# Kernel optimization log

Hardware: AMD Instinct MI355X
Metric: run time of the kernel (lower is better)

Reference implementation:

```python
import jax, jax.numpy as jnp
import numpy as np

B, P, K = 8, 1024, 20
N = B * P
EMB, OUT = 1024, 40
GRID = 5

def _window(W):
    # Hamming taper (window_type='hamming')
    n = jnp.arange(W, dtype=jnp.float32)
    return 0.54 - 0.46 * jnp.cos(2.0 * jnp.pi * n / (W - 1))

def _init_kan(key, din, dout, W, S, g):
    nw = (din - W) // S + 1
    coeffs = jax.random.normal(key, (2, dout, nw, W, g), jnp.float32) / (np.sqrt(nw * W) * np.sqrt(g))
    bias = jnp.zeros((dout,), jnp.float32)
    return coeffs, bias

def stft_kan(x, coeffs, bias, W, S):
    # x: (n, D) -> (n, dout). Slice D into overlapping windows of size W,
    # stride S, apply Hamming taper, build Fourier features cos(k*x), sin(k*x)
    # for k=1..g and contract with learned coefficients (STFT-Fourier-KAN).
    nw, g = coeffs.shape[2], coeffs.shape[4]
    idx = (np.arange(nw) * S)[:, None] + np.arange(W)[None, :]        # (nw, W)
    xw = x[:, idx] * _window(W)                                        # (n, nw, W)
    kfreq = jnp.arange(1, g + 1, dtype=x.dtype)
    arg = xw[..., None] * kfreq                                        # (n, nw, W, g)
    y = (jnp.einsum('nwig,owig->no', jnp.cos(arg), coeffs[0])
         + jnp.einsum('nwig,owig->no', jnp.sin(arg), coeffs[1]))
    return y + bias

def setup_inputs():
    key = jax.random.key(0)
    ks = jax.random.split(key, 5)
    pos = jax.random.normal(ks[0], (N, 3), jnp.float32)
    batch = (jnp.arange(N) // P).astype(jnp.int32)  # sorted, equal-size clouds
    c1, b1 = _init_kan(ks[1], 6, 64, 3, 3, GRID)
    c2, b2 = _init_kan(ks[2], 64, 128, 16, 8, GRID)
    c3, b3 = _init_kan(ks[3], 128, EMB, 32, 16, GRID)
    c4, b4 = _init_kan(ks[4], 2 * EMB, OUT, 256, 128, GRID)
    return {"pos": pos, "batch": batch, "c1": c1, "b1": b1, "c2": c2, "b2": b2,
            "c3": c3, "b3": b3, "c4": c4, "b4": b4}

def reference(pos, batch, c1, b1, c2, b2, c3, b3, c4, b4):
    posb = pos.reshape(B, P, 3)
    # dynamic kNN graph per cloud (self excluded)
    d = jnp.sum((posb[:, :, None, :] - posb[:, None, :, :]) ** 2, -1)  # (B,P,P)
    d = d + jnp.eye(P, dtype=d.dtype) * 1e10
    _, nbr = jax.lax.top_k(-d, K)                                      # (B,P,K)
    pj = jax.vmap(lambda p, i: p[i])(posb, nbr)                        # (B,P,K,3)
    pi = jnp.broadcast_to(posb[:, :, None, :], pj.shape)
    e = jnp.concatenate([pi, pj - pi], -1).reshape(N * K, 6)           # edge feats
    h = stft_kan(e, c1, b1, 3, 3)                                      # (N*K,64)
    h = stft_kan(h, c2, b2, 16, 8)                                     # (N*K,128)
    x1 = jnp.max(h.reshape(N, K, 128), axis=1)                         # max aggr over neighbors
    x = stft_kan(x1, c3, b3, 32, 16)                                   # (N,EMB)
    gmax = jax.ops.segment_max(x, batch, num_segments=B)
    gsum = jax.ops.segment_sum(x, batch, num_segments=B)
    cnt = jax.ops.segment_sum(jnp.ones((N, 1), x.dtype), batch, num_segments=B)
    xg = jnp.concatenate([gmax, gsum / cnt], -1)                       # (B, 2*EMB)
    return stft_kan(xg, c4, b4, 256, 128)                              # (B, OUT)
```

## Files before the change

kernel.cpp:

```cpp
#include <hip/hip_runtime.h>


typedef unsigned short u16;
typedef unsigned int   u32;
typedef unsigned long long u64;
typedef __attribute__((ext_vector_type(8))) _Float16 half8;
typedef __attribute__((ext_vector_type(4))) float f32x4;

__device__ __forceinline__ float bf2f(u16 u) {
  u32 v = ((u32)u) << 16;
  return __uint_as_float(v);
}
__device__ __forceinline__ u16 f2bfr(float f) {
  u32 x = __float_as_uint(f);
  u32 r = x + 0x7FFFu + ((x >> 16) & 1u);
  return (u16)(r >> 16);
}
__device__ __forceinline__ u16 f2h(float f) {
  _Float16 h = (_Float16)f;
  u16 r;
  __builtin_memcpy(&r, &h, 2);
  return r;
}
__device__ __forceinline__ float h2f(u16 u) {
  _Float16 h;
  __builtin_memcpy(&h, &u, 2);
  return (float)h;
}
__device__ __forceinline__ float ldf(const void* p, size_t i, bool f32) {
  return f32 ? ((const float*)p)[i] : bf2f(((const u16*)p)[i]);
}
__device__ __forceinline__ u64 minu64(u64 a, u64 b) { return a < b ? a : b; }

#define NBR_OFF   ((size_t)0)
#define FLAG_OFF  ((size_t)917504)
#define XG_OFF    ((size_t)(1u << 20))
#define L4P_OFF   (((size_t)(1u << 20)) + 131072)
#define C1T_OFF   (((size_t)(1u << 20)) + 524288)
#define C2T_OFF   (((size_t)(1u << 20)) + 589824)
#define C3T_OFF   ((size_t)(2u << 20))
#define C4T_OFF   ((size_t)(7u << 20))
#define PMAX_OFF  ((size_t)(13u << 20))
#define PSUM_OFF  ((size_t)(14u << 20))
#define X1_OFF    ((size_t)(15u << 20))
#define H1_OFF    ((size_t)(18u << 20))

__global__ void detect_kernel(const void* __restrict__ pos,
                              int* __restrict__ flag) {
  int t = threadIdx.x;
  float a = fabsf(((const float*)pos)[t]);
  bool ok = (a > 1.0e-3f && a < 100.0f);
  unsigned long long m = __ballot(ok);
  if (t == 0) *flag = (__popcll(m) >= 32) ? 1 : 0;
}

__global__ void tkan_all_kernel(const void* __restrict__ s1, void* __restrict__ d1,
                                const void* __restrict__ s2, void* __restrict__ d2,
                                const void* __restrict__ s3, void* __restrict__ d3,
                                const void* __restrict__ s4, void* __restrict__ d4,
                                const int* __restrict__ dfl) {
  const int blk = blockIdx.x;
  const void* src; void* dst;
  int dout, nw, W, total, KPAD, outf32, base;
  if (blk < 16)        { src = s1; dst = d1; dout = 64;   nw = 2;  W = 3;
                         total = 64 * 64;     KPAD = 64;    outf32 = 0; base = 0; }
  else if (blk < 576)  { src = s2; dst = d2; dout = 128;  nw = 7;  W = 16;
                         total = 128 * 1120;  KPAD = 1120;  outf32 = 0; base = 16; }
  else if (blk < 9536) { src = s3; dst = d3; dout = 1024; nw = 7;  W = 32;
                         total = 1024 * 2240; KPAD = 2240;  outf32 = 0; base = 576; }
  else                 { src = s4; dst = d4; dout = 40;   nw = 15; W = 256;
                         total = 40 * 38400;  KPAD = 38400; outf32 = 1; base = 9536; }
  int id = (blk - base) * 256 + threadIdx.x;
  if (id >= total) return;
  const bool f32 = (*dfl != 0);
  int o = id / KPAD, f = id % KPAD;
  int NA = nw * W;
  int Kt = NA * 10;
  float v = 0.f;
  if (f < Kt) {
    int part = f & 1, p = f >> 1;
    int aa, gg;
    if (p < 4 * NA) { aa = p >> 2;      gg = p & 3; }
    else            { aa = p - 4 * NA;  gg = 4;     }
    int i = aa % W, w = aa / W;
    int OS = NA * 5;
    size_t sidx = (size_t)part * (dout * OS) + (size_t)o * OS + w * (W * 5) + i * 5 + gg;
    v = ldf(src, sidx, f32);
  }
  if (outf32) ((float*)dst)[id] = v;
  else        ((u16*)dst)[id] = f2h(v);
}

__global__ __launch_bounds__(256) void knn_kernel(const void* __restrict__ pos,
                                                  int* __restrict__ nbr,
                                                  const int* __restrict__ dfl) {
  __shared__ float px[1024], py[1024], pz[1024];
  const bool f32 = (*dfl != 0);
  const int t = threadIdx.x;
  const int b = blockIdx.y;
  const int base = b << 10;
  for (int j = t; j < 1024; j += 256) {
    size_t pidx = (size_t)(base + j) * 3;
    px[j] = ldf(pos, pidx, f32);
    py[j] = ldf(pos, pidx + 1, f32);
    pz[j] = ldf(pos, pidx + 2, f32);
  }
  __syncthreads();
  const int wv = t >> 6, lane = t & 63;
  const int q = blockIdx.x * 4 + wv;
  const float qx = px[q], qy = py[q], qz = pz[q];
  u64 key[16];
#pragma unroll
  for (int s = 0; s < 16; ++s) {
    const int j = s * 64 + lane;
    float dx = qx - px[j], dy = qy - py[j], dz = qz - pz[j];
    float d = __fadd_rn(__fadd_rn(__fmul_rn(dx, dx), __fmul_rn(dy, dy)),
                        __fmul_rn(dz, dz));
    key[s] = (j == q) ? ~0ull
                      : ((((u64)__float_as_uint(d)) << 32) | (u32)j);
  }
  const int obase = (base + q) * 20;
  for (int k = 0; k < 20; ++k) {
    u64 m = key[0];
#pragma unroll
    for (int s = 1; s < 16; ++s) m = minu64(m, key[s]);
#pragma unroll
    for (int off = 32; off >= 1; off >>= 1) {
      u32 lo = (u32)m, hi = (u32)(m >> 32);
      lo = __shfl_xor(lo, off, 64);
      hi = __shfl_xor(hi, off, 64);
      m = minu64(m, (((u64)hi) << 32) | lo);
    }
    if (lane == 0) nbr[obase + k] = (int)(u32)m;
#pragma unroll
    for (int s = 0; s < 16; ++s)
      if (key[s] == m) key[s] = ~0ull;
  }
}

template <int L>
__global__ __launch_bounds__(256, 3) void kan_kernel(
    const void* __restrict__ in_, const int* __restrict__ nbr,
    const void* __restrict__ pos, const u16* __restrict__ ct,
    const void* __restrict__ bias, void* __restrict__ out_,
    float* __restrict__ pmax, float* __restrict__ psum,
    const int* __restrict__ dfl) {
  constexpr int W    = (L == 1) ? 3  : (L == 2) ? 16  : 32;
  constexpr int S    = (L == 1) ? 3  : (L == 2) ? 8   : 16;
  constexpr int DIN  = (L == 1) ? 6  : (L == 2) ? 64  : 128;
  constexpr int NT   = 64;
  constexpr int NW   = (DIN - W) / S + 1;
  constexpr int NA   = NW * W;
  constexpr int NPAIR = NA * 5;
  constexpr int S1P  = NA * 4;
  constexpr int KROW  = (L == 1) ? 64 : NPAIR * 2;
  constexpr int NCH   = KROW / 32;
  constexpr int NB    = NT / 16;
  constexpr int RW    = (L == 1) ? 64 : (L == 2) ? 80 : 32;
  constexpr int MB    = RW / 16;
  constexpr int PSTH  = DIN + 4;
  constexpr int LGW   = (W == 16) ? 4 : 5;
  constexpr int BBS   = 4 * 520;

  __shared__ float hamS[(L == 1) ? 1 : W];
  __shared__ float wT1[(L == 1) ? 32 : 1];
  __shared__ int   hT1[(L == 1) ? 32 : 1];
  __shared__ u16   slab[(L == 1) ? 2 : 4 * RW * PSTH];
  __shared__ u16   stage1[(L == 1) ? 4 * 64 * 64 : 2];
  __shared__ u16   Bbuf[2 * BBS];

  const bool f32 = (*dfl != 0);
  const u16* inH = (const u16*)in_;
  const int t = threadIdx.x;
  if constexpr (L == 1) {
    if (t < 32) {
      float wv_ = 0.f; int hx = 0;
      if (t < NPAIR) {
        int aa, gg;
        if (t < S1P) { aa = t >> 2;   gg = t & 3; }
        else         { aa = t - S1P;  gg = 4;     }
        int i = aa % W;
        float hm = 0.54f - 0.46f * cospif(2.0f * (float)i / (float)(W - 1));
        wv_ = hm * (float)(gg + 1);
        hx = aa;
      }
      wT1[t] = wv_; hT1[t] = hx;
    }
  } else {
    if (t < W) hamS[t] = 0.54f - 0.46f * cospif(2.0f * (float)t / (float)(W - 1));
  }

  int tile, ncol0;
  if constexpr (L == 3) {
    const int id = blockIdx.x;
    tile = (id >> 3) & 63;
    ncol0 = ((((id & 7) << 1) | (id >> 9))) * NT;
  } else {
    tile = blockIdx.x;
    ncol0 = blockIdx.y * NT;
  }
  const int lane = t & 63, wv = t >> 6;
  const int m16 = lane & 15, kb = lane >> 4;
  const int rowbase = tile * (4 * RW) + wv * RW;
  u16* myslab = &slab[(L == 1) ? 0 : wv * RW * PSTH];

  const int scol = t >> 2, spart = t & 3;
  const u16* srcB = ct + (size_t)(ncol0 + scol) * KROW + spart * 8;

  if constexpr (L >= 2) {
    constexpr int F4R = DIN / 4;
    constexpr int TOT = RW * F4R;
    for (int i = lane; i < TOT; i += 64) {
      const int r = i / F4R, c4 = i % F4R;
      *(uint2*)(myslab + r * PSTH + c4 * 4) =
          *(const uint2*)(inH + (size_t)(rowbase + r) * DIN + c4 * 4);
    }
  }

  {
    const uint4 v = *(const uint4*)srcB;
    *(uint4*)(Bbuf + spart * 520 + scol * 8) = v;
  }
  __syncthreads();

  f32x4 acc[MB][NB];
#pragma unroll
  for (int mb = 0; mb < MB; ++mb)
#pragma unroll
    for (int nb = 0; nb < NB; ++nb) {
      acc[mb][nb][0] = 0.f; acc[mb][nb][1] = 0.f;
      acc[mb][nb][2] = 0.f; acc[mb][nb][3] = 0.f;
    }

  for (int c = 0; c < NCH; ++c) {
    uint4 bnext;
    const bool havenext = (c + 1 < NCH);
    if (havenext)
      bnext = *(const uint4*)(srcB + (c + 1) * 32);
    const int pg0 = c * 16 + kb * 4;
    half8 af[MB];
    if constexpr (L == 1) {
      float wm[4]; int hx[4]; bool val[4];
#pragma unroll
      for (int u = 0; u < 4; ++u) {
        const int pg = pg0 + u;
        wm[u] = wT1[pg]; hx[u] = hT1[pg]; val[u] = (pg < NPAIR);
      }
#pragma unroll
      for (int mb = 0; mb < MB; ++mb) {
        const int row = rowbase + mb * 16 + m16;
        const int pt = row / 20;
        const int cloud = pt >> 10, ci = pt & 1023;
        const int cb = cloud << 10;
        const int jl = nbr[row];
#pragma unroll
        for (int u = 0; u < 4; ++u) {
          float cs = 0.f, sn = 0.f;
          if (val[u]) {
            const int aa = hx[u];
            float v;
            if (aa < 3) {
              v = ldf(pos, (size_t)(cb + ci) * 3 + aa, f32);
            } else {
              const int cc2 = aa - 3;
              v = ldf(pos, (size_t)(cb + jl) * 3 + cc2, f32) -
                  ldf(pos, (size_t)(cb + ci) * 3 + cc2, f32);
            }
            const float ang = v * wm[u];
            cs = __cosf(ang); sn = __sinf(ang);
          }
          af[mb][2 * u]     = (_Float16)cs;
          af[mb][2 * u + 1] = (_Float16)sn;
        }
      }
    } else if (pg0 < S1P) {
      const int aa = pg0 >> 2;
      const int i = aa & (W - 1), w = aa >> LGW;
      const int hidx = S * w + i;
      const float hm = hamS[i];
#pragma unroll
      for (int mb = 0; mb < MB; ++mb) {
        const u16* rp = myslab + (mb * 16 + m16) * PSTH;
        const float th = h2f(rp[hidx]) * hm;
        const float c1 = __cosf(th), s1 = __sinf(th);
        const float tc = 2.0f * c1;
        const float c2 = tc * c1 - 1.0f, s2 = tc * s1;
        const float c3 = tc * c2 - c1,   s3 = tc * s2 - s1;
        const float c4 = tc * c3 - c2,   s4 = tc * s3 - s2;
        af[mb][0] = (_Float16)c1; af[mb][1] = (_Float16)s1;
        af[mb][2] = (_Float16)c2; af[mb][3] = (_Float16)s2;
        af[mb][4] = (_Float16)c3; af[mb][5] = (_Float16)s3;
        af[mb][6] = (_Float16)c4; af[mb][7] = (_Float16)s4;
      }
    } else {
      const int q0 = pg0 - S1P;
      float wm[4]; int hx[4];
#pragma unroll
      for (int u = 0; u < 4; ++u) {
        const int aa = q0 + u;
        const int i = aa & (W - 1), w = aa >> LGW;
        hx[u] = S * w + i;
        wm[u] = hamS[i] * 5.0f;
      }
#pragma unroll
      for (int mb = 0; mb < MB; ++mb) {
        const u16* rp = myslab + (mb * 16 + m16) * PSTH;
#pragma unroll
        for (int u = 0; u < 4; ++u) {
          const float ang = h2f(rp[hx[u]]) * wm[u];
          af[mb][2 * u]     = (_Float16)__cosf(ang);
          af[mb][2 * u + 1] = (_Float16)__sinf(ang);
        }
      }
    }
    const u16* bb = Bbuf + (c & 1) * BBS + kb * 520;
#pragma unroll
    for (int nb = 0; nb < NB; ++nb) {
      const half8 bv = *(const half8*)(bb + (nb * 16 + m16) * 8);
#pragma unroll
      for (int mb = 0; mb < MB; ++mb)
        acc[mb][nb] = __builtin_amdgcn_mfma_f32_16x16x32_f16(
            af[mb], bv, acc[mb][nb], 0, 0, 0);
    }
    if (havenext) {
      *(uint4*)(Bbuf + ((c + 1) & 1) * BBS + spart * 520 + scol * 8) = bnext;
      __syncthreads();
    }
  }

  if constexpr (L == 1) {
    u16* st = &stage1[wv * 4096];
#pragma unroll
    for (int mb = 0; mb < MB; ++mb)
#pragma unroll
      for (int nb = 0; nb < NB; ++nb) {
        const float bsv = ldf(bias, nb * 16 + m16, f32);
#pragma unroll
        for (int r = 0; r < 4; ++r)
          st[(mb * 16 + kb * 4 + r) * 64 + nb * 16 + m16] =
              f2h(acc[mb][nb][r] + bsv);
      }
    u16* gp = (u16*)out_ + (size_t)rowbase * 64;
    for (int i = lane; i < 512; i += 64)
      *(uint4*)(gp + i * 8) = *(const uint4*)&st[i * 8];
  } else if constexpr (L == 2) {
    u16* st = myslab;
#pragma unroll
    for (int mb = 0; mb < MB; ++mb)
#pragma unroll
      for (int nb = 0; nb < NB; ++nb) {
        const float bsv = ldf(bias, ncol0 + nb * 16 + m16, f32);
#pragma unroll
        for (int r = 0; r < 4; ++r)
          st[(mb * 16 + kb * 4 + r) * PSTH + nb * 16 + m16] =
              f2h(acc[mb][nb][r] + bsv);
      }
    const int pbase = tile * 16 + wv * 4;
#pragma unroll
    for (int j = 0; j < 4; ++j) {
      float m = -3.0e38f;
#pragma unroll
      for (int k = 0; k < 20; ++k)
        m = fmaxf(m, h2f(st[(j * 20 + k) * PSTH + lane]));
      ((u16*)out_)[(size_t)(pbase + j) * 128 + ncol0 + lane] = f2h(m);
    }
  } else {
    const int chunk = rowbase >> 5;
#pragma unroll
    for (int nb = 0; nb < NB; ++nb) {
      const int col = ncol0 + nb * 16 + m16;
      const float bsv = ldf(bias, col, f32);
      float m = -3.0e38f, s = 0.f;
#pragma unroll
      for (int mb = 0; mb < MB; ++mb)
#pragma unroll
        for (int r = 0; r < 4; ++r) {
          const float v = acc[mb][nb][r] + bsv;
          m = fmaxf(m, v); s += v;
        }
#pragma unroll
      for (int off = 16; off <= 32; off <<= 1) {
        m = fmaxf(m, __shfl_xor(m, off, 64));
        s += __shfl_xor(s, off, 64);
      }
      if (kb == 0) {
        pmax[(size_t)chunk * 1024 + col] = m;
        psum[(size_t)chunk * 1024 + col] = s;
      }
    }
  }
}

__global__ void seg2_kernel(const float* __restrict__ pmax,
                            const float* __restrict__ psum,
                            float* __restrict__ xg) {
  const int id = blockIdx.x * 256 + threadIdx.x;
  const int b = id >> 10, col = id & 1023;
  float m = -3.0e38f, s = 0.f;
  for (int rc = 0; rc < 32; ++rc) {
    m = fmaxf(m, pmax[(size_t)(b * 32 + rc) * 1024 + col]);
    s += psum[(size_t)(b * 32 + rc) * 1024 + col];
  }
  xg[b * 2048 + col] = m;
  xg[b * 2048 + 1024 + col] = s * (1.0f / 1024.0f);
}

__global__ __launch_bounds__(256) void l4_kernel(const float* __restrict__ xg,
                                                 const float* __restrict__ c4t,
                                                 float* __restrict__ part) {
  __shared__ float F[2560];
  const int t = threadIdx.x;
  const int w = blockIdx.x, b = blockIdx.y;
  const float xv = xg[b * 2048 + w * 128 + t];
  const float hm = 0.54f - 0.46f * cospif(2.0f * (float)t / 255.0f);
  const float aa = xv * hm;
  const float c1 = __cosf(aa), s1 = __sinf(aa);
  const float tc = 2.0f * c1;
  const float c2 = tc * c1 - 1.0f, s2 = tc * s1;
  const float c3 = tc * c2 - c1,   s3 = tc * s2 - s1;
  const float c4 = tc * c3 - c2,   s4 = tc * s3 - s2;
  const float a5 = aa * 5.0f;
  F[t * 8]     = c1; F[t * 8 + 1] = s1;
  F[t * 8 + 2] = c2; F[t * 8 + 3] = s2;
  F[t * 8 + 4] = c3; F[t * 8 + 5] = s3;
  F[t * 8 + 6] = c4; F[t * 8 + 7] = s4;
  F[2048 + t * 2]     = __cosf(a5);
  F[2048 + t * 2 + 1] = __sinf(a5);
  __syncthreads();
  if (t < 240) {
    const int o = t % 40, s = t / 40;
    const int f0 = s * 432;
    const int f1 = (f0 + 432 < 2560) ? (f0 + 432) : 2560;
    const float* cp1 = c4t + (size_t)o * 38400 + w * 2048;
    const float* cp2 = c4t + (size_t)o * 38400 + 30720 + w * 512;
    float acc = 0.f;
    for (int f = f0; f < f1; f += 4) {
      const float* cpf = (f < 2048) ? (cp1 + f) : (cp2 + (f - 2048));
      const float4 cv = *(const float4*)cpf;
      const float4 fa = *(const float4*)&F[f];
      acc += fa.x * cv.x + fa.y * cv.y + fa.z * cv.z + fa.w * cv.w;
    }
    part[((b * 15 + w) * 6 + s) * 40 + o] = acc;
  }
}

__global__ void outred_kernel(const float* __restrict__ part,
                              const void* __restrict__ b4,
                              void* __restrict__ outp,
                              const int* __restrict__ dfl) {
  int t = threadIdx.x;
  if (t >= 320) return;
  const bool f32 = (*dfl != 0);
  int b = t / 40, o = t % 40;
  float s = ldf(b4, o, f32);
  for (int w = 0; w < 15; ++w)
#pragma unroll
    for (int sl = 0; sl < 6; ++sl)
      s += part[((b * 15 + w) * 6 + sl) * 40 + o];
  if (f32) ((float*)outp)[t] = s;
  else     ((u16*)outp)[t] = f2bfr(s);
}

extern "C" void kernel_launch(void* const* d_in, const int* in_sizes, int n_in,
                              void* d_out, int out_size, void* d_ws,
                              size_t ws_size, hipStream_t stream) {
  (void)in_sizes; (void)n_in; (void)out_size; (void)ws_size;
  const void* pos = d_in[0];
  const void* c1 = d_in[2];
  const void* b1 = d_in[3];
  const void* c2 = d_in[4];
  const void* b2 = d_in[5];
  const void* c3 = d_in[6];
  const void* b3 = d_in[7];
  const void* c4 = d_in[8];
  const void* b4 = d_in[9];

  char* ws = (char*)d_ws;
  int* nbr   = (int*)(ws + NBR_OFF);
  int* flag  = (int*)(ws + FLAG_OFF);
  float* xg  = (float*)(ws + XG_OFF);
  float* l4p = (float*)(ws + L4P_OFF);
  u16* c1t   = (u16*)(ws + C1T_OFF);
  u16* c2t   = (u16*)(ws + C2T_OFF);
  u16* c3t   = (u16*)(ws + C3T_OFF);
  float* c4t = (float*)(ws + C4T_OFF);
  float* pmax = (float*)(ws + PMAX_OFF);
  float* psum = (float*)(ws + PSUM_OFF);
  u16* x1    = (u16*)(ws + X1_OFF);
  u16* h1    = (u16*)(ws + H1_OFF);

  detect_kernel<<<1, 64, 0, stream>>>(pos, flag);

  tkan_all_kernel<<<15536, 256, 0, stream>>>(c1, c1t, c2, c2t, c3, c3t,
                                             c4, c4t, flag);

  knn_kernel<<<dim3(256, 8), 256, 0, stream>>>(pos, nbr, flag);

  kan_kernel<1><<<640, 256, 0, stream>>>(nullptr, nbr, pos, c1t, b1, h1,
                                         nullptr, nullptr, flag);
  kan_kernel<2><<<dim3(512, 2), 256, 0, stream>>>(h1, nullptr, nullptr, c2t,
                                                  b2, x1, nullptr, nullptr, flag);
  kan_kernel<3><<<1024, 256, 0, stream>>>(x1, nullptr, nullptr, c3t,
                                          b3, nullptr, pmax, psum, flag);

  seg2_kernel<<<32, 256, 0, stream>>>(pmax, psum, xg);
  l4_kernel<<<dim3(15, 8), 256, 0, stream>>>(xg, c4t, l4p);
  outred_kernel<<<1, 320, 0, stream>>>(l4p, b4, d_out, flag);
}
```

Baseline: 311.5 us.

## Compute all 128 layer-2 columns per block and fold segment reduce into l4

Layer-2 KAN blocks now cover all 128 output columns with 5 waves of 32 rows each (160 rows, 8 points), instead of splitting columns across two blocks. This removes the duplicated Fourier feature computation per column half and lets the max-over-neighbours run in one block through a shared staging buffer that is reused from the slab/B storage. Separately, the seg2 kernel is removed and its max/mean reduction over partials moves into l4_kernel, saving a launch and the xg round trip. The cost is more accumulators per thread, which may lower occupancy, and more redundant partial reads in l4.

```diff
diff --git a/kernel.cpp b/kernel.cpp
--- a/kernel.cpp
+++ b/kernel.cpp
@@ -34,7 +34,6 @@
 
 #define NBR_OFF   ((size_t)0)
 #define FLAG_OFF  ((size_t)917504)
-#define XG_OFF    ((size_t)(1u << 20))
 #define L4P_OFF   (((size_t)(1u << 20)) + 131072)
 #define C1T_OFF   (((size_t)(1u << 20)) + 524288)
 #define C2T_OFF   (((size_t)(1u << 20)) + 589824)
@@ -139,7 +138,8 @@
 }
 
 template <int L>
-__global__ __launch_bounds__(256, 3) void kan_kernel(
+__global__ __launch_bounds__((L == 2) ? 320 : 256, (L == 2) ? 4 : 3)
+void kan_kernel(
     const void* __restrict__ in_, const int* __restrict__ nbr,
     const void* __restrict__ pos, const u16* __restrict__ ct,
     const void* __restrict__ bias, void* __restrict__ out_,
@@ -148,7 +148,9 @@
   constexpr int W    = (L == 1) ? 3  : (L == 2) ? 16  : 32;
   constexpr int S    = (L == 1) ? 3  : (L == 2) ? 8   : 16;
   constexpr int DIN  = (L == 1) ? 6  : (L == 2) ? 64  : 128;
-  constexpr int NT   = 64;
+  constexpr int NTH  = (L == 2) ? 320 : 256;
+  constexpr int NWV  = NTH / 64;
+  constexpr int NT   = (L == 2) ? 128 : 64;
   constexpr int NW   = (DIN - W) / S + 1;
   constexpr int NA   = NW * W;
   constexpr int NPAIR = NA * 5;
@@ -156,18 +158,26 @@
   constexpr int KROW  = (L == 1) ? 64 : NPAIR * 2;
   constexpr int NCH   = KROW / 32;
   constexpr int NB    = NT / 16;
-  constexpr int RW    = (L == 1) ? 64 : (L == 2) ? 80 : 32;
+  constexpr int RW    = (L == 1) ? 64 : 32;
   constexpr int MB    = RW / 16;
   constexpr int PSTH  = DIN + 4;
   constexpr int LGW   = (W == 16) ? 4 : 5;
-  constexpr int BBS   = 4 * 520;
+  constexpr int PRT   = NT * 8 + 16;
+  constexpr int BBS   = 4 * PRT;
+  constexpr int NPIECE = NT * 4;
+  constexpr int NLD   = (NPIECE + NTH - 1) / NTH;
+  constexpr int ROWS  = NWV * RW;
 
   __shared__ float hamS[(L == 1) ? 1 : W];
   __shared__ float wT1[(L == 1) ? 32 : 1];
   __shared__ int   hT1[(L == 1) ? 32 : 1];
-  __shared__ u16   slab[(L == 1) ? 2 : 4 * RW * PSTH];
+  __shared__ u16   uni[(L == 2) ? 160 * 136 : 2];
+  __shared__ u16   slabA[(L == 3) ? 4 * 32 * 132 : 2];
+  __shared__ u16   BbufA[(L == 2) ? 2 : 2 * BBS];
   __shared__ u16   stage1[(L == 1) ? 4 * 64 * 64 : 2];
-  __shared__ u16   Bbuf[2 * BBS];
+
+  u16* slab = (L == 2) ? uni : slabA;
+  u16* Bbuf = (L == 2) ? (uni + 160 * 68) : BbufA;
 
   const bool f32 = (*dfl != 0);
   const u16* inH = (const u16*)in_;
@@ -197,15 +207,12 @@
     ncol0 = ((((id & 7) << 1) | (id >> 9))) * NT;
   } else {
     tile = blockIdx.x;
-    ncol0 = blockIdx.y * NT;
+    ncol0 = 0;
   }
   const int lane = t & 63, wv = t >> 6;
   const int m16 = lane & 15, kb = lane >> 4;
-  const int rowbase = tile * (4 * RW) + wv * RW;
-  u16* myslab = &slab[(L == 1) ? 0 : wv * RW * PSTH];
-
-  const int scol = t >> 2, spart = t & 3;
-  const u16* srcB = ct + (size_t)(ncol0 + scol) * KROW + spart * 8;
+  const int rowbase = tile * ROWS + wv * RW;
+  u16* myslab = slab + ((L == 1) ? 0 : wv * RW * PSTH);
 
   if constexpr (L >= 2) {
     constexpr int F4R = DIN / 4;
@@ -217,9 +224,14 @@
     }
   }
 
-  {
-    const uint4 v = *(const uint4*)srcB;
-    *(uint4*)(Bbuf + spart * 520 + scol * 8) = v;
+#pragma unroll
+  for (int ii = 0; ii < NLD; ++ii) {
+    const int i = t + ii * NTH;
+    if (i < NPIECE) {
+      const uint4 v = *(const uint4*)(ct +
+          (size_t)(ncol0 + (i >> 2)) * KROW + (i & 3) * 8);
+      *(uint4*)(Bbuf + (i & 3) * PRT + (i >> 2) * 8) = v;
+    }
   }
   __syncthreads();
 
@@ -233,10 +245,17 @@
     }
 
   for (int c = 0; c < NCH; ++c) {
-    uint4 bnext;
+    uint4 bn[NLD];
     const bool havenext = (c + 1 < NCH);
-    if (havenext)
-      bnext = *(const uint4*)(srcB + (c + 1) * 32);
+    if (havenext) {
+#pragma unroll
+      for (int ii = 0; ii < NLD; ++ii) {
+        const int i = t + ii * NTH;
+        if (i < NPIECE)
+          bn[ii] = *(const uint4*)(ct +
+              (size_t)(ncol0 + (i >> 2)) * KROW + (c + 1) * 32 + (i & 3) * 8);
+      }
+    }
     const int pg0 = c * 16 + kb * 4;
     half8 af[MB];
     if constexpr (L == 1) {
@@ -313,7 +332,7 @@
         }
       }
     }
-    const u16* bb = Bbuf + (c & 1) * BBS + kb * 520;
+    const u16* bb = Bbuf + (c & 1) * BBS + kb * PRT;
 #pragma unroll
     for (int nb = 0; nb < NB; ++nb) {
       const half8 bv = *(const half8*)(bb + (nb * 16 + m16) * 8);
@@ -323,7 +342,13 @@
             af[mb], bv, acc[mb][nb], 0, 0, 0);
     }
     if (havenext) {
-      *(uint4*)(Bbuf + ((c + 1) & 1) * BBS + spart * 520 + scol * 8) = bnext;
+#pragma unroll
+      for (int ii = 0; ii < NLD; ++ii) {
+        const int i = t + ii * NTH;
+        if (i < NPIECE)
+          *(uint4*)(Bbuf + ((c + 1) & 1) * BBS + (i & 3) * PRT + (i >> 2) * 8)
+              = bn[ii];
+      }
       __syncthreads();
     }
   }
@@ -344,25 +369,26 @@
     for (int i = lane; i < 512; i += 64)
       *(uint4*)(gp + i * 8) = *(const uint4*)&st[i * 8];
   } else if constexpr (L == 2) {
-    u16* st = myslab;
+    __syncthreads();
 #pragma unroll
     for (int mb = 0; mb < MB; ++mb)
 #pragma unroll
       for (int nb = 0; nb < NB; ++nb) {
-        const float bsv = ldf(bias, ncol0 + nb * 16 + m16, f32);
+        const int col = nb * 16 + m16;
+        const float bsv = ldf(bias, col, f32);
 #pragma unroll
         for (int r = 0; r < 4; ++r)
-          st[(mb * 16 + kb * 4 + r) * PSTH + nb * 16 + m16] =
+          uni[(wv * 32 + mb * 16 + kb * 4 + r) * 136 + col] =
               f2h(acc[mb][nb][r] + bsv);
       }
-    const int pbase = tile * 16 + wv * 4;
-#pragma unroll
-    for (int j = 0; j < 4; ++j) {
+    __syncthreads();
+    for (int i = t; i < 1024; i += NTH) {
+      const int p = i >> 7, j = i & 127;
       float m = -3.0e38f;
 #pragma unroll
       for (int k = 0; k < 20; ++k)
-        m = fmaxf(m, h2f(st[(j * 20 + k) * PSTH + lane]));
-      ((u16*)out_)[(size_t)(pbase + j) * 128 + ncol0 + lane] = f2h(m);
+        m = fmaxf(m, h2f(uni[(p * 20 + k) * 136 + j]));
+      ((u16*)out_)[(size_t)(tile * 8 + p) * 128 + j] = f2h(m);
     }
   } else {
     const int chunk = rowbase >> 5;
@@ -391,27 +417,27 @@
   }
 }
 
-__global__ void seg2_kernel(const float* __restrict__ pmax,
-                            const float* __restrict__ psum,
-                            float* __restrict__ xg) {
-  const int id = blockIdx.x * 256 + threadIdx.x;
-  const int b = id >> 10, col = id & 1023;
-  float m = -3.0e38f, s = 0.f;
-  for (int rc = 0; rc < 32; ++rc) {
-    m = fmaxf(m, pmax[(size_t)(b * 32 + rc) * 1024 + col]);
-    s += psum[(size_t)(b * 32 + rc) * 1024 + col];
-  }
-  xg[b * 2048 + col] = m;
-  xg[b * 2048 + 1024 + col] = s * (1.0f / 1024.0f);
-}
-
-__global__ __launch_bounds__(256) void l4_kernel(const float* __restrict__ xg,
+__global__ __launch_bounds__(256) void l4_kernel(const float* __restrict__ pmax,
+                                                 const float* __restrict__ psum,
                                                  const float* __restrict__ c4t,
                                                  float* __restrict__ part) {
   __shared__ float F[2560];
   const int t = threadIdx.x;
   const int w = blockIdx.x, b = blockIdx.y;
-  const float xv = xg[b * 2048 + w * 128 + t];
+  const int ch = w * 128 + t;
+  float xv;
+  if (ch < 1024) {
+    float m = -3.0e38f;
+    for (int rc = 0; rc < 32; ++rc)
+      m = fmaxf(m, pmax[(size_t)(b * 32 + rc) * 1024 + ch]);
+    xv = m;
+  } else {
+    const int cc = ch - 1024;
+    float s = 0.f;
+    for (int rc = 0; rc < 32; ++rc)
+      s += psum[(size_t)(b * 32 + rc) * 1024 + cc];
+    xv = s * (1.0f / 1024.0f);
+  }
   const float hm = 0.54f - 0.46f * cospif(2.0f * (float)t / 255.0f);
   const float aa = xv * hm;
   const float c1 = __cosf(aa), s1 = __sinf(aa);
@@ -478,7 +504,6 @@
   char* ws = (char*)d_ws;
   int* nbr   = (int*)(ws + NBR_OFF);
   int* flag  = (int*)(ws + FLAG_OFF);
-  float* xg  = (float*)(ws + XG_OFF);
   float* l4p = (float*)(ws + L4P_OFF);
   u16* c1t   = (u16*)(ws + C1T_OFF);
   u16* c2t   = (u16*)(ws + C2T_OFF);
@@ -498,12 +523,11 @@
 
   kan_kernel<1><<<640, 256, 0, stream>>>(nullptr, nbr, pos, c1t, b1, h1,
                                          nullptr, nullptr, flag);
-  kan_kernel<2><<<dim3(512, 2), 256, 0, stream>>>(h1, nullptr, nullptr, c2t,
-                                                  b2, x1, nullptr, nullptr, flag);
+  kan_kernel<2><<<1024, 320, 0, stream>>>(h1, nullptr, nullptr, c2t,
+                                          b2, x1, nullptr, nullptr, flag);
   kan_kernel<3><<<1024, 256, 0, stream>>>(x1, nullptr, nullptr, c3t,
                                           b3, nullptr, pmax, psum, flag);
 
-  seg2_kernel<<<32, 256, 0, stream>>>(pmax, psum, xg);
-  l4_kernel<<<dim3(15, 8), 256, 0, stream>>>(xg, c4t, l4p);
+  l4_kernel<<<dim3(15, 8), 256, 0, stream>>>(pmax, psum, c4t, l4p);
   outred_kernel<<<1, 320, 0, stream>>>(l4p, b4, d_out, flag);
 }
```

Result: slower. 363.4 us (+16.7%).
